# Kernel optimization log

Measured on AMD Instinct MI355X. Metric: run time of the kernel, lower is better.

The kernel has to match this reference:

```python
import jax, jax.numpy as jnp
import numpy as np

B, T, V = 8, 2048, 1024


def setup_inputs() -> dict:
    key = jax.random.key(0)
    k1, k2, k3, k4, k5 = jax.random.split(key, 5)
    idx = jax.random.randint(k1, (B, T), 0, V)
    # nn.Embedding(length, 1) weight, std=0.02
    v = 0.02 * jax.random.normal(k2, (T, 1), dtype=jnp.float32)
    # nn.Linear(V, V, bias=False) weights (torch layout: out x in), std=0.02
    Wk = 0.02 * jax.random.normal(k3, (V, V), dtype=jnp.float32)
    Wq = 0.02 * jax.random.normal(k4, (V, V), dtype=jnp.float32)
    Wv = 0.02 * jax.random.normal(k5, (V, V), dtype=jnp.float32)
    return {"idx": idx, "v": v, "Wk": Wk, "Wq": Wq, "Wv": Wv}


def reference(idx, v, Wk, Wq, Wv):
    Tn = v.shape[0]
    Vn = Wk.shape[0]
    # one-hot token embedding [B, T, V]
    e = jax.nn.one_hot(idx, Vn, dtype=jnp.float32)
    # relative positions, clipped at 0; pos_embd[i, j] = v[i-j] for i >= j else 0
    pos = jnp.arange(Tn)
    rel = jnp.clip(pos[:, None] - pos[None, :], 0)
    pos_embd = jnp.tril(v[rel, 0])  # [T, T]
    # layer_one = pos_embd @ e  -> [B, T, V]
    layer_one = jnp.einsum('ts,bsv->btv', pos_embd, e)
    K = layer_one @ Wk.T           # Linear: x @ W^T
    Q = e @ Wq.T
    attention = jnp.einsum('btv,bsv->bts', Q, K)  # [B, T, T]
    causal = jnp.tril(jnp.ones((Tn, Tn), dtype=bool))
    masked_attention = jnp.where(causal, attention, 0.0)
    output = jnp.einsum('bts,bsv->btv', masked_attention, e @ Wv.T)
    logits = output + 0.001
    return logits
```

## Files before the change

### kernel.cpp

```cpp
#include <hip/hip_runtime.h>
#include <stdint.h>

#define T_DIM 2048
#define V_DIM 1024
#define B_DIM 8
#define NT 16

typedef unsigned int u32;
typedef unsigned short u16;
typedef unsigned char u8;
typedef __attribute__((ext_vector_type(8))) short s16x8;
typedef __attribute__((ext_vector_type(4))) float f32x4;

__device__ __forceinline__ u16 f2bf(float x) {
  u32 u = __builtin_bit_cast(u32, x);
  u = u + 0x7FFFu + ((u >> 16) & 1u);
  return (u16)(u >> 16);
}

#define GLD16(gp, lp) __builtin_amdgcn_global_load_lds( \
    (const __attribute__((address_space(1))) u32*)(gp), \
    (__attribute__((address_space(3))) u32*)(lp), 16, 0, 0)

__device__ const u8 TRIL_ORD[72] = {
  127, 119,
  126, 118, 110,  102,
  125, 117, 109, 101, 93,  85,
  124, 116, 108, 100, 92, 84, 76,  68,
  123, 115, 107, 99, 91, 83, 75, 67, 59,  51,
  122, 114, 106, 98, 90, 82, 74, 66, 58, 50, 42,  34,
  121, 113, 105, 97, 89, 81, 73, 65, 57, 49, 41, 33, 25,  17,
  120, 112, 104, 96, 88, 80, 72, 64, 56, 48, 40, 32, 24, 16, 8,  0
};

template<int MODE, bool F32OUT>
__global__ void __launch_bounds__(256, 2)
gemm_bt(const u16* __restrict__ A, int lda, long long batchA,
        const u16* __restrict__ Bt, int ldb, long long batchB,
        void* __restrict__ Cv, int ldc, long long batchC,
        int K, float bias)
{
  int bn, bm, bz;
  if (MODE == 0) {
    bn = blockIdx.x; bm = blockIdx.y; bz = blockIdx.z;
  } else if (MODE == 1) {
    int lam = blockIdx.x;
    int j = (lam < 256) ? lam : (lam < 512 ? 767 - lam : lam);
    int tau = j >> 3; bz = j & 7;
    int pk = TRIL_ORD[tau]; bm = pk >> 3; bn = pk & 7;
  } else {
    int lam = blockIdx.x;
    int rr2 = lam & 255;
    int zq = rr2 >> 5;
    bn = (rr2 >> 3) & 3;
    bz = rr2 & 7;
    bm = (lam < 256) ? 15 - zq : zq;
  }
  const u16* Ab = A + (long long)bz * batchA;
  const u16* Bb = Bt + (long long)bz * batchB;
  int m0 = bm * 128, n0 = bn * 256;
  int kmax = K;
  if (MODE == 1) {
    int kl1 = (bm + 1) * 128, kl2 = (bn + 1) * 256;
    int kl = kl1 < kl2 ? kl1 : kl2;
    kmax = kl < K ? kl : K;
  }
  if (MODE == 2) { int kl = (bm + 1) * 128; kmax = kl < K ? kl : K; }

  __shared__ u16 As[128 * 64];
  __shared__ u16 Bs[256 * 64];

  int tid = threadIdx.x;
  int lane = tid & 63;
  int wid = tid >> 6;
  int wm = wid >> 1, wn = wid & 1;

  f32x4 acc[4][8] = {};

  int r0 = tid >> 3;
  int gcol = (((tid & 7) - r0) & 7) * 8;
  const u16* ga = Ab + (long long)(m0 + r0) * lda + gcol;
  const u16* gb = Bb + (long long)(n0 + r0) * ldb + gcol;
  u16* la = As + tid * 8;
  u16* lb = Bs + tid * 8;
  long long lda32 = (long long)32 * lda;
  long long ldb32 = (long long)32 * ldb;

  int rm = lane & 15;
  int q = lane >> 4;

  for (int k0 = 0; k0 < kmax; k0 += 64) {
#pragma unroll
    for (int i = 0; i < 4; i++)
      GLD16(ga + k0 + i * lda32, la + i * 2048);
#pragma unroll
    for (int i = 0; i < 8; i++)
      GLD16(gb + k0 + i * ldb32, lb + i * 2048);
    __syncthreads();
#pragma unroll
    for (int ks = 0; ks < 2; ks++) {
      s16x8 af[4], bfv[8];
#pragma unroll
      for (int mi = 0; mi < 4; mi++) {
        int row = wm * 64 + mi * 16 + rm;
        int p = ((ks * 4 + q) + row) & 7;
        af[mi] = *(const s16x8*)&As[row * 64 + p * 8];
      }
#pragma unroll
      for (int ni = 0; ni < 8; ni++) {
        int row = wn * 128 + ni * 16 + rm;
        int p = ((ks * 4 + q) + row) & 7;
        bfv[ni] = *(const s16x8*)&Bs[row * 64 + p * 8];
      }
#pragma unroll
      for (int mi = 0; mi < 4; mi++)
#pragma unroll
        for (int ni = 0; ni < 8; ni++)
          acc[mi][ni] = __builtin_amdgcn_mfma_f32_16x16x32_bf16(
              af[mi], bfv[ni], acc[mi][ni], 0, 0, 0);
    }
    __syncthreads();
  }

  int col = lane & 15;
  int rq = (lane >> 4) * 4;
#pragma unroll
  for (int mi = 0; mi < 4; mi++) {
#pragma unroll
    for (int ni = 0; ni < 8; ni++) {
      int lr = wm * 64 + mi * 16 + rq;
      int lc = wn * 128 + ni * 16 + col;
#pragma unroll
      for (int rr = 0; rr < 4; rr++) {
        float val = acc[mi][ni][rr];
        if (MODE == 1 && (n0 + lc) > (m0 + lr + rr)) val = 0.f;
        long long off = (long long)(m0 + lr + rr) * ldc + (n0 + lc);
        if (F32OUT) {
          float* C = (float*)Cv + (long long)bz * batchC;
          C[off] = val + bias;
        } else {
          u16* C = (u16*)Cv + (long long)bz * batchC;
          C[off] = f2bf(val);
        }
      }
    }
  }
}

__global__ void transpose_cast2(const float* __restrict__ s0, u16* __restrict__ d0,
                                const float* __restrict__ s1, u16* __restrict__ d1)
{
  const float* src = blockIdx.z ? s1 : s0;
  u16* dst = blockIdx.z ? d1 : d0;
  __shared__ float tile[32][33];
  int x0 = blockIdx.x * 32, y0 = blockIdx.y * 32;
  int tx = threadIdx.x, ty = threadIdx.y;
#pragma unroll
  for (int k = 0; k < 4; k++)
    tile[ty + k * 8][tx] = src[(long long)(y0 + ty + k * 8) * V_DIM + x0 + tx];
  __syncthreads();
#pragma unroll
  for (int k = 0; k < 4; k++)
    dst[(long long)(x0 + ty + k * 8) * V_DIM + y0 + tx] = f2bf(tile[tx][ty + k * 8]);
}

__global__ void cast_bf16(const float* __restrict__ src, u16* __restrict__ dst)
{
  int i = blockIdx.x * 1024 + threadIdx.x;
#pragma unroll
  for (int k = 0; k < 4; k++) dst[i + k * 256] = f2bf(src[i + k * 256]);
}

__global__ void build_p(const float* __restrict__ v, u16* __restrict__ P)
{
  int gid = blockIdx.x * 256 + threadIdx.x;
  int e0 = gid * 8;
  int s = e0 >> 11, u0 = e0 & 2047;
  s16x8 o;
#pragma unroll
  for (int k = 0; k < 8; k++) {
    int u = u0 + k;
    o[k] = (short)((u <= s) ? f2bf(v[s - u]) : (u16)0);
  }
  *(s16x8*)&P[e0] = o;
}

__global__ void __launch_bounds__(256)
gather_g(const int* __restrict__ idx, const u16* __restrict__ Mb,
         u16* __restrict__ G, int b0)
{
  int t = blockIdx.x, z = blockIdx.y;
  const int* idxrow = idx + (long long)(b0 + z) * T_DIM;
  __shared__ u16 Mrow[V_DIM];
  int tid = threadIdx.x;
  int rowid = idxrow[t];
  const u32* src = (const u32*)(Mb + (long long)rowid * V_DIM);
  u32* dstl = (u32*)Mrow;
  dstl[tid] = src[tid];
  dstl[tid + 256] = src[tid + 256];
  __syncthreads();
  int u0 = tid * 8;
  int4 i0 = *(const int4*)&idxrow[u0];
  int4 i1 = *(const int4*)&idxrow[u0 + 4];
  s16x8 o;
  o[0] = (short)Mrow[i0.x]; o[1] = (short)Mrow[i0.y];
  o[2] = (short)Mrow[i0.z]; o[3] = (short)Mrow[i0.w];
  o[4] = (short)Mrow[i1.x]; o[5] = (short)Mrow[i1.y];
  o[6] = (short)Mrow[i1.z]; o[7] = (short)Mrow[i1.w];
  *(s16x8*)&G[((long long)z * T_DIM + t) * T_DIM + u0] = o;
}

__global__ void __launch_bounds__(256)
gather_y(const int* __restrict__ idx, const u16* __restrict__ Wvb,
         u16* __restrict__ Yt, int b0)
{
  int j = blockIdx.x, z = blockIdx.y;
  const int* idxrow = idx + (long long)(b0 + z) * T_DIM;
  __shared__ u16 Wrow[V_DIM];
  int tid = threadIdx.x;
  const u32* src = (const u32*)(Wvb + (long long)j * V_DIM);
  u32* dstl = (u32*)Wrow;
  dstl[tid] = src[tid];
  dstl[tid + 256] = src[tid + 256];
  __syncthreads();
  int s0 = tid * 8;
  int4 i0 = *(const int4*)&idxrow[s0];
  int4 i1 = *(const int4*)&idxrow[s0 + 4];
  s16x8 o;
  o[0] = (short)Wrow[i0.x]; o[1] = (short)Wrow[i0.y];
  o[2] = (short)Wrow[i0.z]; o[3] = (short)Wrow[i0.w];
  o[4] = (short)Wrow[i1.x]; o[5] = (short)Wrow[i1.y];
  o[6] = (short)Wrow[i1.z]; o[7] = (short)Wrow[i1.w];
  *(s16x8*)&Yt[((long long)z * V_DIM + j) * T_DIM + s0] = o;
}

extern "C" void kernel_launch(void* const* d_in, const int* in_sizes, int n_in,
                              void* d_out, int out_size, void* d_ws, size_t ws_size,
                              hipStream_t stream)
{
  const int*   idx = (const int*)d_in[0];
  const float* v   = (const float*)d_in[1];
  const float* Wk  = (const float*)d_in[2];
  const float* Wq  = (const float*)d_in[3];
  const float* Wv  = (const float*)d_in[4];
  float* out = (float*)d_out;

  char* p = (char*)d_ws;
  const size_t SZ_VV = (size_t)V_DIM * V_DIM * 2;
  const size_t SZ_TT = (size_t)T_DIM * T_DIM * 2;
  const size_t SZ_VT = (size_t)V_DIM * T_DIM * 2;
  u16* WqT = (u16*)p; p += SZ_VV;
  u16* WkT = (u16*)p; p += SZ_VV;
  u16* Wvb = (u16*)p; p += SZ_VV;
  u16* Mb  = (u16*)p; p += SZ_VV;
  u16* P   = (u16*)p; p += SZ_TT;
  size_t used = (size_t)(p - (char*)d_ws);
  size_t per = 2 * SZ_TT + SZ_VT;
  int nb = 8;
  while (nb > 1 && used + (size_t)nb * per > ws_size) nb >>= 1;
  u16* G    = (u16*)p; p += (size_t)nb * SZ_TT;
  u16* Abuf = (u16*)p; p += (size_t)nb * SZ_TT;
  u16* Yt   = (u16*)p;

  transpose_cast2<<<dim3(32, 32, 2), dim3(32, 8), 0, stream>>>(Wq, WqT, Wk, WkT);
  cast_bf16<<<1024, 256, 0, stream>>>(Wv, Wvb);
  build_p<<<2048, 256, 0, stream>>>(v, P);
  gemm_bt<0, false><<<dim3(V_DIM / 256, V_DIM / 128, 1), 256, 0, stream>>>(
      WqT, V_DIM, 0, WkT, V_DIM, 0, Mb, V_DIM, 0, V_DIM, 0.f);

  for (int b0 = 0; b0 < B_DIM; b0 += nb) {
    gather_g<<<dim3(T_DIM, nb), 256, 0, stream>>>(idx, Mb, G, b0);
    gather_y<<<dim3(V_DIM, nb), 256, 0, stream>>>(idx, Wvb, Yt, b0);
    gemm_bt<1, false><<<dim3(nb * 72, 1, 1), 256, 0, stream>>>(
        G, T_DIM, (long long)T_DIM * T_DIM, P, T_DIM, 0,
        Abuf, T_DIM, (long long)T_DIM * T_DIM, T_DIM, 0.f);
    gemm_bt<2, true><<<dim3((V_DIM / 256) * nb * NT, 1, 1), 256, 0, stream>>>(
        Abuf, T_DIM, (long long)T_DIM * T_DIM, Yt, T_DIM, (long long)V_DIM * T_DIM,
        out + (long long)b0 * T_DIM * V_DIM, V_DIM, (long long)T_DIM * V_DIM,
        T_DIM, 0.001f);
  }
}
```

Baseline: 236.6 us.

## Shrink GEMM tiles to 128x128 and merge prep and gather kernels

Reduces the GEMM tile from 128x256 to 128x128, which halves the accumulators and shared memory per block and doubles the block count. The causal MODE 1 schedule now enumerates the 136 lower-triangular 128x128 tiles with a loop instead of a lookup table, and MODE 2 orders blocks from heaviest to lightest row. The weight transpose and cast kernels are fused into one launch, as are the two gather kernels. Smaller tiles lower per-block operand reuse and raise total global traffic, in exchange for finer causal skipping and better load balance.

Result: faster. 205.4 us (-13.2%).

```diff
diff --git a/kernel.cpp b/kernel.cpp
--- a/kernel.cpp
+++ b/kernel.cpp
@@ -8,7 +8,6 @@
 
 typedef unsigned int u32;
 typedef unsigned short u16;
-typedef unsigned char u8;
 typedef __attribute__((ext_vector_type(8))) short s16x8;
 typedef __attribute__((ext_vector_type(4))) float f32x4;
 
@@ -21,17 +20,6 @@
 #define GLD16(gp, lp) __builtin_amdgcn_global_load_lds( \
     (const __attribute__((address_space(1))) u32*)(gp), \
     (__attribute__((address_space(3))) u32*)(lp), 16, 0, 0)
-
-__device__ const u8 TRIL_ORD[72] = {
-  127, 119,
-  126, 118, 110,  102,
-  125, 117, 109, 101, 93,  85,
-  124, 116, 108, 100, 92, 84, 76,  68,
-  123, 115, 107, 99, 91, 83, 75, 67, 59,  51,
-  122, 114, 106, 98, 90, 82, 74, 66, 58, 50, 42,  34,
-  121, 113, 105, 97, 89, 81, 73, 65, 57, 49, 41, 33, 25,  17,
-  120, 112, 104, 96, 88, 80, 72, 64, 56, 48, 40, 32, 24, 16, 8,  0
-};
 
 template<int MODE, bool F32OUT>
 __global__ void __launch_bounds__(256, 2)
@@ -45,37 +33,32 @@
     bn = blockIdx.x; bm = blockIdx.y; bz = blockIdx.z;
   } else if (MODE == 1) {
     int lam = blockIdx.x;
-    int j = (lam < 256) ? lam : (lam < 512 ? 767 - lam : lam);
-    int tau = j >> 3; bz = j & 7;
-    int pk = TRIL_ORD[tau]; bm = pk >> 3; bn = pk & 7;
+    int tau = lam >> 3; bz = lam & 7;
+    int b = NT - 1, off = 0;
+    while (tau >= off + (NT - b)) { off += NT - b; b--; }
+    bn = b; bm = b + (tau - off);
   } else {
     int lam = blockIdx.x;
-    int rr2 = lam & 255;
-    int zq = rr2 >> 5;
-    bn = (rr2 >> 3) & 3;
-    bz = rr2 & 7;
-    bm = (lam < 256) ? 15 - zq : zq;
+    bm = (NT - 1) - (lam >> 6);
+    bn = (lam >> 3) & 7;
+    bz = lam & 7;
   }
   const u16* Ab = A + (long long)bz * batchA;
   const u16* Bb = Bt + (long long)bz * batchB;
-  int m0 = bm * 128, n0 = bn * 256;
+  int m0 = bm * 128, n0 = bn * 128;
   int kmax = K;
-  if (MODE == 1) {
-    int kl1 = (bm + 1) * 128, kl2 = (bn + 1) * 256;
-    int kl = kl1 < kl2 ? kl1 : kl2;
-    kmax = kl < K ? kl : K;
-  }
+  if (MODE == 1) { int kl = (bn + 1) * 128; kmax = kl < K ? kl : K; }
   if (MODE == 2) { int kl = (bm + 1) * 128; kmax = kl < K ? kl : K; }
 
   __shared__ u16 As[128 * 64];
-  __shared__ u16 Bs[256 * 64];
+  __shared__ u16 Bs[128 * 64];
 
   int tid = threadIdx.x;
   int lane = tid & 63;
   int wid = tid >> 6;
   int wm = wid >> 1, wn = wid & 1;
 
-  f32x4 acc[4][8] = {};
+  f32x4 acc[4][4] = {};
 
   int r0 = tid >> 3;
   int gcol = (((tid & 7) - r0) & 7) * 8;
@@ -94,12 +77,12 @@
     for (int i = 0; i < 4; i++)
       GLD16(ga + k0 + i * lda32, la + i * 2048);
 #pragma unroll
-    for (int i = 0; i < 8; i++)
+    for (int i = 0; i < 4; i++)
       GLD16(gb + k0 + i * ldb32, lb + i * 2048);
     __syncthreads();
 #pragma unroll
     for (int ks = 0; ks < 2; ks++) {
-      s16x8 af[4], bfv[8];
+      s16x8 af[4], bfv[4];
 #pragma unroll
       for (int mi = 0; mi < 4; mi++) {
         int row = wm * 64 + mi * 16 + rm;
@@ -107,15 +90,15 @@
         af[mi] = *(const s16x8*)&As[row * 64 + p * 8];
       }
 #pragma unroll
-      for (int ni = 0; ni < 8; ni++) {
-        int row = wn * 128 + ni * 16 + rm;
+      for (int ni = 0; ni < 4; ni++) {
+        int row = wn * 64 + ni * 16 + rm;
         int p = ((ks * 4 + q) + row) & 7;
         bfv[ni] = *(const s16x8*)&Bs[row * 64 + p * 8];
       }
 #pragma unroll
       for (int mi = 0; mi < 4; mi++)
 #pragma unroll
-        for (int ni = 0; ni < 8; ni++)
+        for (int ni = 0; ni < 4; ni++)
           acc[mi][ni] = __builtin_amdgcn_mfma_f32_16x16x32_bf16(
               af[mi], bfv[ni], acc[mi][ni], 0, 0, 0);
     }
@@ -127,9 +110,9 @@
 #pragma unroll
   for (int mi = 0; mi < 4; mi++) {
 #pragma unroll
-    for (int ni = 0; ni < 8; ni++) {
+    for (int ni = 0; ni < 4; ni++) {
       int lr = wm * 64 + mi * 16 + rq;
-      int lc = wn * 128 + ni * 16 + col;
+      int lc = wn * 64 + ni * 16 + col;
 #pragma unroll
       for (int rr = 0; rr < 4; rr++) {
         float val = acc[mi][ni][rr];
@@ -147,11 +130,20 @@
   }
 }
 
-__global__ void transpose_cast2(const float* __restrict__ s0, u16* __restrict__ d0,
-                                const float* __restrict__ s1, u16* __restrict__ d1)
-{
-  const float* src = blockIdx.z ? s1 : s0;
-  u16* dst = blockIdx.z ? d1 : d0;
+__global__ void prep_weights(const float* __restrict__ Wq, u16* __restrict__ WqT,
+                             const float* __restrict__ Wk, u16* __restrict__ WkT,
+                             const float* __restrict__ Wv, u16* __restrict__ Wvb)
+{
+  int z = blockIdx.z;
+  if (z == 2) {
+    int bx = blockIdx.y * 32 + blockIdx.x;
+    int i = bx * 1024 + threadIdx.y * 32 + threadIdx.x;
+#pragma unroll
+    for (int k = 0; k < 4; k++) Wvb[i + k * 256] = f2bf(Wv[i + k * 256]);
+    return;
+  }
+  const float* src = z ? Wk : Wq;
+  u16* dst = z ? WkT : WqT;
   __shared__ float tile[32][33];
   int x0 = blockIdx.x * 32, y0 = blockIdx.y * 32;
   int tx = threadIdx.x, ty = threadIdx.y;
@@ -162,13 +154,6 @@
 #pragma unroll
   for (int k = 0; k < 4; k++)
     dst[(long long)(x0 + ty + k * 8) * V_DIM + y0 + tx] = f2bf(tile[tx][ty + k * 8]);
-}
-
-__global__ void cast_bf16(const float* __restrict__ src, u16* __restrict__ dst)
-{
-  int i = blockIdx.x * 1024 + threadIdx.x;
-#pragma unroll
-  for (int k = 0; k < 4; k++) dst[i + k * 256] = f2bf(src[i + k * 256]);
 }
 
 __global__ void build_p(const float* __restrict__ v, u16* __restrict__ P)
@@ -186,40 +171,24 @@
 }
 
 __global__ void __launch_bounds__(256)
-gather_g(const int* __restrict__ idx, const u16* __restrict__ Mb,
-         u16* __restrict__ G, int b0)
-{
-  int t = blockIdx.x, z = blockIdx.y;
+gather_gy(const int* __restrict__ idx, const u16* __restrict__ Mb,
+          const u16* __restrict__ Wvb, u16* __restrict__ G,
+          u16* __restrict__ Yt, int b0)
+{
+  int bx = blockIdx.x, z = blockIdx.y;
   const int* idxrow = idx + (long long)(b0 + z) * T_DIM;
-  __shared__ u16 Mrow[V_DIM];
+  __shared__ u16 Row[V_DIM];
   int tid = threadIdx.x;
-  int rowid = idxrow[t];
-  const u32* src = (const u32*)(Mb + (long long)rowid * V_DIM);
-  u32* dstl = (u32*)Mrow;
-  dstl[tid] = src[tid];
-  dstl[tid + 256] = src[tid + 256];
-  __syncthreads();
-  int u0 = tid * 8;
-  int4 i0 = *(const int4*)&idxrow[u0];
-  int4 i1 = *(const int4*)&idxrow[u0 + 4];
-  s16x8 o;
-  o[0] = (short)Mrow[i0.x]; o[1] = (short)Mrow[i0.y];
-  o[2] = (short)Mrow[i0.z]; o[3] = (short)Mrow[i0.w];
-  o[4] = (short)Mrow[i1.x]; o[5] = (short)Mrow[i1.y];
-  o[6] = (short)Mrow[i1.z]; o[7] = (short)Mrow[i1.w];
-  *(s16x8*)&G[((long long)z * T_DIM + t) * T_DIM + u0] = o;
-}
-
-__global__ void __launch_bounds__(256)
-gather_y(const int* __restrict__ idx, const u16* __restrict__ Wvb,
-         u16* __restrict__ Yt, int b0)
-{
-  int j = blockIdx.x, z = blockIdx.y;
-  const int* idxrow = idx + (long long)(b0 + z) * T_DIM;
-  __shared__ u16 Wrow[V_DIM];
-  int tid = threadIdx.x;
-  const u32* src = (const u32*)(Wvb + (long long)j * V_DIM);
-  u32* dstl = (u32*)Wrow;
+  const u32* src;
+  u16* dst;
+  if (bx < T_DIM) {
+    src = (const u32*)(Mb + (long long)idxrow[bx] * V_DIM);
+    dst = G + ((long long)z * T_DIM + bx) * T_DIM;
+  } else {
+    src = (const u32*)(Wvb + (long long)(bx - T_DIM) * V_DIM);
+    dst = Yt + ((long long)z * V_DIM + (bx - T_DIM)) * T_DIM;
+  }
+  u32* dstl = (u32*)Row;
   dstl[tid] = src[tid];
   dstl[tid + 256] = src[tid + 256];
   __syncthreads();
@@ -227,11 +196,11 @@
   int4 i0 = *(const int4*)&idxrow[s0];
   int4 i1 = *(const int4*)&idxrow[s0 + 4];
   s16x8 o;
-  o[0] = (short)Wrow[i0.x]; o[1] = (short)Wrow[i0.y];
-  o[2] = (short)Wrow[i0.z]; o[3] = (short)Wrow[i0.w];
-  o[4] = (short)Wrow[i1.x]; o[5] = (short)Wrow[i1.y];
-  o[6] = (short)Wrow[i1.z]; o[7] = (short)Wrow[i1.w];
-  *(s16x8*)&Yt[((long long)z * V_DIM + j) * T_DIM + s0] = o;
+  o[0] = (short)Row[i0.x]; o[1] = (short)Row[i0.y];
+  o[2] = (short)Row[i0.z]; o[3] = (short)Row[i0.w];
+  o[4] = (short)Row[i1.x]; o[5] = (short)Row[i1.y];
+  o[6] = (short)Row[i1.z]; o[7] = (short)Row[i1.w];
+  *(s16x8*)&dst[s0] = o;
 }
 
 extern "C" void kernel_launch(void* const* d_in, const int* in_sizes, int n_in,
@@ -262,19 +231,17 @@
   u16* Abuf = (u16*)p; p += (size_t)nb * SZ_TT;
   u16* Yt   = (u16*)p;
 
-  transpose_cast2<<<dim3(32, 32, 2), dim3(32, 8), 0, stream>>>(Wq, WqT, Wk, WkT);
-  cast_bf16<<<1024, 256, 0, stream>>>(Wv, Wvb);
+  prep_weights<<<dim3(32, 32, 3), dim3(32, 8), 0, stream>>>(Wq, WqT, Wk, WkT, Wv, Wvb);
   build_p<<<2048, 256, 0, stream>>>(v, P);
-  gemm_bt<0, false><<<dim3(V_DIM / 256, V_DIM / 128, 1), 256, 0, stream>>>(
+  gemm_bt<0, false><<<dim3(V_DIM / 128, V_DIM / 128, 1), 256, 0, stream>>>(
       WqT, V_DIM, 0, WkT, V_DIM, 0, Mb, V_DIM, 0, V_DIM, 0.f);
 
   for (int b0 = 0; b0 < B_DIM; b0 += nb) {
-    gather_g<<<dim3(T_DIM, nb), 256, 0, stream>>>(idx, Mb, G, b0);
-    gather_y<<<dim3(V_DIM, nb), 256, 0, stream>>>(idx, Wvb, Yt, b0);
-    gemm_bt<1, false><<<dim3(nb * 72, 1, 1), 256, 0, stream>>>(
+    gather_gy<<<dim3(T_DIM + V_DIM, nb), 256, 0, stream>>>(idx, Mb, Wvb, G, Yt, b0);
+    gemm_bt<1, false><<<dim3(nb * 136, 1, 1), 256, 0, stream>>>(
         G, T_DIM, (long long)T_DIM * T_DIM, P, T_DIM, 0,
         Abuf, T_DIM, (long long)T_DIM * T_DIM, T_DIM, 0.f);
-    gemm_bt<2, true><<<dim3((V_DIM / 256) * nb * NT, 1, 1), 256, 0, stream>>>(
+    gemm_bt<2, true><<<dim3((V_DIM / 128) * nb * NT, 1, 1), 256, 0, stream>>>(
         Abuf, T_DIM, (long long)T_DIM * T_DIM, Yt, T_DIM, (long long)V_DIM * T_DIM,
         out + (long long)b0 * T_DIM * V_DIM, V_DIM, (long long)T_DIM * V_DIM,
         T_DIM, 0.001f);
```
